# Performance work log

Hardware: AMD Instinct MI355X
Metric: run time of the kernel (lower is better)

Reference implementation:

```python
import jax, jax.numpy as jnp
import numpy as np

N, E, B = 50000, 640000, 4
H, L = 128, 4
NODE_IN, EDGE_IN, COND_IN, NODE_OUT = 12, 4, 10, 3


def _mlp(x, w1, b1, w2, b2):
    # Linear -> ReLU -> Linear
    return jnp.maximum(x @ w1 + b1, 0.0) @ w2 + b2


def setup_inputs() -> dict:
    key = jax.random.key(0)
    keys = iter(jax.random.split(key, 64))

    def p(*shape):
        fan_in = shape[-2] if len(shape) >= 2 else shape[-1]
        return (jax.random.normal(next(keys), shape, jnp.float32) / np.sqrt(fan_in)).astype(jnp.float32)

    inp = {
        "x": jax.random.normal(next(keys), (N, NODE_IN), jnp.float32),
        "edge_index": jax.random.randint(next(keys), (2, E), 0, N),
        "edge_attr": jax.random.normal(next(keys), (E, EDGE_IN), jnp.float32),
        "conditions": jax.random.normal(next(keys), (B, COND_IN), jnp.float32),
        "batch": jnp.sort(jax.random.randint(next(keys), (N,), 0, B)),
        # encoders
        "enc_node_w1": p(NODE_IN, H), "enc_node_b1": jnp.zeros((H,), jnp.float32),
        "enc_node_w2": p(H, H), "enc_node_b2": jnp.zeros((H,), jnp.float32),
        "enc_edge_w1": p(EDGE_IN, H), "enc_edge_b1": jnp.zeros((H,), jnp.float32),
        "enc_edge_w2": p(H, H), "enc_edge_b2": jnp.zeros((H,), jnp.float32),
        "enc_cond_w1": p(COND_IN, H), "enc_cond_b1": jnp.zeros((H,), jnp.float32),
        "enc_cond_w2": p(H, H), "enc_cond_b2": jnp.zeros((H,), jnp.float32),
        # shared MultiheadAttention: with a single key, softmax weight == 1 per head,
        # so output = out_proj(v_proj(kv)); q/k projections cancel exactly (and have
        # identically zero gradient), so only v/out projections are materialized.
        "attn_wv": p(H, H), "attn_bv": jnp.zeros((H,), jnp.float32),
        "attn_wo": p(H, H), "attn_bo": jnp.zeros((H,), jnp.float32),
        # processor layers (stacked over L)
        "pe_w1": p(L, 4 * H, H), "pe_b1": jnp.zeros((L, H), jnp.float32),
        "pe_w2": p(L, H, H), "pe_b2": jnp.zeros((L, H), jnp.float32),
        "pn_w1": p(L, 3 * H, H), "pn_b1": jnp.zeros((L, H), jnp.float32),
        "pn_w2": p(L, H, H), "pn_b2": jnp.zeros((L, H), jnp.float32),
        # decoder
        "dec_w1": p(H, H), "dec_b1": jnp.zeros((H,), jnp.float32),
        "dec_w2": p(H, NODE_OUT), "dec_b2": jnp.zeros((NODE_OUT,), jnp.float32),
    }
    return inp


def reference(x, edge_index, edge_attr, conditions, batch,
              enc_node_w1, enc_node_b1, enc_node_w2, enc_node_b2,
              enc_edge_w1, enc_edge_b1, enc_edge_w2, enc_edge_b2,
              enc_cond_w1, enc_cond_b1, enc_cond_w2, enc_cond_b2,
              attn_wv, attn_bv, attn_wo, attn_bo,
              pe_w1, pe_b1, pe_w2, pe_b2,
              pn_w1, pn_b1, pn_w2, pn_b2,
              dec_w1, dec_b1, dec_w2, dec_b2):
    n = x.shape[0]
    h = _mlp(x, enc_node_w1, enc_node_b1, enc_node_w2, enc_node_b2)           # [N,H]
    e = _mlp(edge_attr, enc_edge_w1, enc_edge_b1, enc_edge_w2, enc_edge_b2)   # [E,H]
    u = _mlp(conditions, enc_cond_w1, enc_cond_b1, enc_cond_w2, enc_cond_b2)  # [B,H]

    row, col = edge_index[0], edge_index[1]
    u_nodes = u[batch]                                                        # [N,H]
    # single-key cross-attention -> softmax over 1 key == 1 -> out_proj(v_proj(u))
    x_cond = (u_nodes @ attn_wv + attn_bv) @ attn_wo + attn_bo               # [N,H], same every layer
    u_edges = u_nodes[row]                                                    # u[batch[row]]

    for l in range(pe_w1.shape[0]):
        # edge update: cat([src, dest, edge_attr, u[batch_e]]) -> MLP
        e = _mlp(jnp.concatenate([h[row], h[col], e, u_edges], axis=1),
                 pe_w1[l], pe_b1[l], pe_w2[l], pe_b2[l])
        # scatter-add aggregation (index_add on row)
        agg = jax.ops.segment_sum(e, row, num_segments=n)                     # [N,H]
        # node update with residual
        h = h + _mlp(jnp.concatenate([h, agg, x_cond], axis=1),
                     pn_w1[l], pn_b1[l], pn_w2[l], pn_b2[l])

    return _mlp(h, dec_w1, dec_b1, dec_w2, dec_b2)                            # [N,node_out]
```

## Files before the change

### kernel.cpp

```cpp
#include <hip/hip_runtime.h>
#include <cstddef>

#define NN 50000
#define NNP 50048
#define NE 640000
#define NB 4
#define H  128
#define NL 4
#define TE 64

typedef unsigned int u32;
typedef unsigned short u16;
typedef __attribute__((ext_vector_type(8))) short bf16x8;
typedef __attribute__((ext_vector_type(4))) float f32x4;

__device__ __forceinline__ float bf2f(u16 s) {
    union { u32 u; float f; } v; v.u = ((u32)s) << 16; return v.f;
}
__device__ __forceinline__ u16 f2bf(float f) {
    union { float f; u32 u; } v; v.f = f;
    u32 u = v.u;
    u += 0x7FFF + ((u >> 16) & 1);
    return (u16)(u >> 16);
}
__device__ __forceinline__ void unpack8(uint4 raw, float* d) {
    d[0] = bf2f(raw.x & 0xFFFF); d[1] = bf2f(raw.x >> 16);
    d[2] = bf2f(raw.y & 0xFFFF); d[3] = bf2f(raw.y >> 16);
    d[4] = bf2f(raw.z & 0xFFFF); d[5] = bf2f(raw.z >> 16);
    d[6] = bf2f(raw.w & 0xFFFF); d[7] = bf2f(raw.w >> 16);
}
__device__ __forceinline__ bf16x8 ld_f32_bf8(const float* __restrict__ p) {
    const float4 a = *(const float4*)p;
    const float4 b = *(const float4*)(p + 4);
    bf16x8 r;
    r[0] = (short)f2bf(a.x); r[1] = (short)f2bf(a.y);
    r[2] = (short)f2bf(a.z); r[3] = (short)f2bf(a.w);
    r[4] = (short)f2bf(b.x); r[5] = (short)f2bf(b.y);
    r[6] = (short)f2bf(b.z); r[7] = (short)f2bf(b.w);
    return r;
}

__global__ __launch_bounds__(256) void k_zero(float* __restrict__ p, int n4) {
    const int i = blockIdx.x * 256 + threadIdx.x;
    if (i < n4) ((float4*)p)[i] = make_float4(0.f, 0.f, 0.f, 0.f);
}

__global__ __launch_bounds__(256) void k_prep(
    const float* __restrict__ pe_w1, const float* __restrict__ pe_w2,
    const float* __restrict__ pn_w1, const float* __restrict__ pn_w2,
    const float* __restrict__ ew2,   const float* __restrict__ nw2,
    u16* __restrict__ W1t, u16* __restrict__ W2t,
    u16* __restrict__ WaT, u16* __restrict__ WbT,
    u16* __restrict__ Wn1aT, u16* __restrict__ Wn1bT, u16* __restrict__ Wn2T,
    u16* __restrict__ W2et, u16* __restrict__ W2nt) {
    const int li = blockIdx.x;
    const float* src; u16* dst;
    switch (blockIdx.y) {
        case 0: src = pe_w1 + ((size_t)li * 512 + 256) * H; dst = W1t  + (size_t)li * H * H; break;
        case 1: src = pe_w2 + (size_t)li * H * H;           dst = W2t  + (size_t)li * H * H; break;
        case 2: src = pe_w1 + (size_t)li * 512 * H;         dst = WaT  + (size_t)li * H * H; break;
        case 3: src = pe_w1 + ((size_t)li * 512 + 128) * H; dst = WbT  + (size_t)li * H * H; break;
        case 4: src = pn_w1 + (size_t)li * 384 * H;         dst = Wn1aT + (size_t)li * H * H; break;
        case 5: src = pn_w1 + ((size_t)li * 384 + 128) * H; dst = Wn1bT + (size_t)li * H * H; break;
        case 6: src = pn_w2 + (size_t)li * H * H;           dst = Wn2T + (size_t)li * H * H; break;
        default:
            if (li == 0)      { src = ew2; dst = W2et; }
            else if (li == 1) { src = nw2; dst = W2nt; }
            else return;
            break;
    }
    for (int idx = threadIdx.x; idx < H * H; idx += 256) {
        const int n = idx >> 7, k = idx & 127;
        dst[idx] = f2bf(src[(size_t)k * H + n]);
    }
}

__global__ __launch_bounds__(128) void k_small(
    const float* __restrict__ cond,
    const float* __restrict__ ecw1, const float* __restrict__ ecb1,
    const float* __restrict__ ecw2, const float* __restrict__ ecb2,
    const float* __restrict__ wv, const float* __restrict__ bv,
    const float* __restrict__ wo, const float* __restrict__ bo,
    const float* __restrict__ pe_w1, const float* __restrict__ pe_b1,
    const float* __restrict__ pn_w1, const float* __restrict__ pn_b1,
    float* __restrict__ cbat, float* __restrict__ nbat) {
    __shared__ float tmp[NB][H];
    __shared__ float uL[NB][H];
    __shared__ float xcL[NB][H];
    const int t = threadIdx.x;
    for (int b = 0; b < NB; ++b) {
        float a = ecb1[t];
        for (int k = 0; k < 10; ++k) a = fmaf(cond[b * 10 + k], ecw1[k * H + t], a);
        tmp[b][t] = fmaxf(a, 0.f);
    }
    __syncthreads();
    for (int b = 0; b < NB; ++b) {
        float a = ecb2[t];
        for (int k = 0; k < H; ++k) a = fmaf(tmp[b][k], ecw2[k * H + t], a);
        uL[b][t] = a;
    }
    __syncthreads();
    for (int b = 0; b < NB; ++b) {
        float a = bv[t];
        for (int k = 0; k < H; ++k) a = fmaf(uL[b][k], wv[k * H + t], a);
        tmp[b][t] = a;
    }
    __syncthreads();
    for (int b = 0; b < NB; ++b) {
        float a = bo[t];
        for (int k = 0; k < H; ++k) a = fmaf(tmp[b][k], wo[k * H + t], a);
        xcL[b][t] = a;
    }
    __syncthreads();
    for (int l = 0; l < NL; ++l) {
        const float* w1u = pe_w1 + ((size_t)l * 512 + 384) * H;
        for (int b = 0; b < NB; ++b) {
            float a = pe_b1[l * H + t];
            for (int k = 0; k < H; ++k) a = fmaf(uL[b][k], w1u[k * H + t], a);
            cbat[(l * NB + b) * H + t] = a;
        }
        const float* w1x = pn_w1 + ((size_t)l * 384 + 256) * H;
        for (int b = 0; b < NB; ++b) {
            float a = pn_b1[l * H + t];
            for (int k = 0; k < H; ++k) a = fmaf(xcL[b][k], w1x[k * H + t], a);
            nbat[(l * NB + b) * H + t] = a;
        }
    }
}

__global__ __launch_bounds__(128) void k_dec_n(
    const float* __restrict__ h,
    const float* __restrict__ w1, const float* __restrict__ b1,
    const float* __restrict__ w2, const float* __restrict__ b2,
    float* __restrict__ out) {
    __shared__ float hid[H];
    const int t = threadIdx.x;
    const long long n = blockIdx.x;
    float a = b1[t];
    for (int k = 0; k < H; ++k) a = fmaf(h[n * H + k], w1[k * H + t], a);
    hid[t] = fmaxf(a, 0.f);
    __syncthreads();
    if (t < 3) {
        float v = b2[t];
        for (int k = 0; k < H; ++k) v = fmaf(hid[k], w2[k * 3 + t], v);
        out[n * 3 + t] = v;
    }
}

__global__ __launch_bounds__(256) void k_enc_e_mfma(
    const float* __restrict__ ea,
    const float* __restrict__ w1, const float* __restrict__ b1,
    const u16* __restrict__ W2et, const float* __restrict__ b2,
    u16* __restrict__ e) {
    __shared__ float SI[TE][H + 4];
    const int t = threadIdx.x;
    const long long e0 = (long long)blockIdx.x * TE;
    const int w = t >> 6, l = t & 63;
    const int m16 = l & 15, g = l >> 4;
    const int row = w * 16 + m16;

    const float4 av = *(const float4*)&ea[(size_t)(e0 + row) * 4];

    bf16x8 afrag[4];
#pragma unroll
    for (int ks = 0; ks < 4; ++ks) {
        const int c0 = ks * 32 + g * 8;
        float hv[8];
        {
            const float4 ba = *(const float4*)&b1[c0];
            const float4 bb = *(const float4*)&b1[c0 + 4];
            hv[0] = ba.x; hv[1] = ba.y; hv[2] = ba.z; hv[3] = ba.w;
            hv[4] = bb.x; hv[5] = bb.y; hv[6] = bb.z; hv[7] = bb.w;
        }
#pragma unroll
        for (int k = 0; k < 4; ++k) {
            const float s = (k == 0) ? av.x : (k == 1) ? av.y : (k == 2) ? av.z : av.w;
            const float4 wa = *(const float4*)&w1[k * H + c0];
            const float4 wb = *(const float4*)&w1[k * H + c0 + 4];
            hv[0] = fmaf(s, wa.x, hv[0]); hv[1] = fmaf(s, wa.y, hv[1]);
            hv[2] = fmaf(s, wa.z, hv[2]); hv[3] = fmaf(s, wa.w, hv[3]);
            hv[4] = fmaf(s, wb.x, hv[4]); hv[5] = fmaf(s, wb.y, hv[5]);
            hv[6] = fmaf(s, wb.z, hv[6]); hv[7] = fmaf(s, wb.w, hv[7]);
        }
#pragma unroll
        for (int j = 0; j < 8; ++j) afrag[ks][j] = (short)f2bf(fmaxf(hv[j], 0.f));
    }

    f32x4 acc[8];
#pragma unroll
    for (int nt = 0; nt < 8; ++nt) {
        const float bb = b2[nt * 16 + m16];
        acc[nt][0] = bb; acc[nt][1] = bb; acc[nt][2] = bb; acc[nt][3] = bb;
    }
#pragma unroll
    for (int ks = 0; ks < 4; ++ks) {
#pragma unroll
        for (int nt = 0; nt < 8; ++nt) {
            const bf16x8 bfr =
                *(const bf16x8*)&W2et[(size_t)(nt * 16 + m16) * H + ks * 32 + g * 8];
            acc[nt] = __builtin_amdgcn_mfma_f32_16x16x32_bf16(afrag[ks], bfr, acc[nt], 0, 0, 0);
        }
    }

#pragma unroll
    for (int nt = 0; nt < 8; ++nt)
#pragma unroll
        for (int j = 0; j < 4; ++j)
            SI[w * 16 + g * 4 + j][nt * 16 + m16] = acc[nt][j];
    __syncthreads();
    for (int u = t; u < TE * 16; u += 256) {
        const int j = u >> 4, c8 = (u & 15) * 8;
        const float* sp = &SI[j][c8];
        uint4 pk;
        pk.x = (u32)f2bf(sp[0]) | ((u32)f2bf(sp[1]) << 16);
        pk.y = (u32)f2bf(sp[2]) | ((u32)f2bf(sp[3]) << 16);
        pk.z = (u32)f2bf(sp[4]) | ((u32)f2bf(sp[5]) << 16);
        pk.w = (u32)f2bf(sp[6]) | ((u32)f2bf(sp[7]) << 16);
        *(uint4*)&e[(size_t)(e0 + j) * H + c8] = pk;
    }
}

__global__ __launch_bounds__(256) void k_enc_n_mfma(
    const float* __restrict__ x,
    const float* __restrict__ w1, const float* __restrict__ b1,
    const u16* __restrict__ W2nt, const float* __restrict__ b2,
    float* __restrict__ h) {
    __shared__ float SI[TE][H + 4];
    const int t = threadIdx.x;
    const long long n0 = (long long)blockIdx.x * TE;
    const int w = t >> 6, l = t & 63;
    const int m16 = l & 15, g = l >> 4;
    const int row = w * 16 + m16;
    const long long nr = (n0 + row < NN) ? (n0 + row) : (NN - 1);

    float av[12];
    {
        const float4 a0 = *(const float4*)&x[nr * 12];
        const float4 a1 = *(const float4*)&x[nr * 12 + 4];
        const float4 a2 = *(const float4*)&x[nr * 12 + 8];
        av[0] = a0.x; av[1] = a0.y; av[2] = a0.z; av[3] = a0.w;
        av[4] = a1.x; av[5] = a1.y; av[6] = a1.z; av[7] = a1.w;
        av[8] = a2.x; av[9] = a2.y; av[10] = a2.z; av[11] = a2.w;
    }

    bf16x8 afrag[4];
#pragma unroll
    for (int ks = 0; ks < 4; ++ks) {
        const int c0 = ks * 32 + g * 8;
        float hv[8];
        {
            const float4 ba = *(const float4*)&b1[c0];
            const float4 bb = *(const float4*)&b1[c0 + 4];
            hv[0] = ba.x; hv[1] = ba.y; hv[2] = ba.z; hv[3] = ba.w;
            hv[4] = bb.x; hv[5] = bb.y; hv[6] = bb.z; hv[7] = bb.w;
        }
#pragma unroll
        for (int k = 0; k < 12; ++k) {
            const float s = av[k];
            const float4 wa = *(const float4*)&w1[k * H + c0];
            const float4 wb = *(const float4*)&w1[k * H + c0 + 4];
            hv[0] = fmaf(s, wa.x, hv[0]); hv[1] = fmaf(s, wa.y, hv[1]);
            hv[2] = fmaf(s, wa.z, hv[2]); hv[3] = fmaf(s, wa.w, hv[3]);
            hv[4] = fmaf(s, wb.x, hv[4]); hv[5] = fmaf(s, wb.y, hv[5]);
            hv[6] = fmaf(s, wb.z, hv[6]); hv[7] = fmaf(s, wb.w, hv[7]);
        }
#pragma unroll
        for (int j = 0; j < 8; ++j) afrag[ks][j] = (short)f2bf(fmaxf(hv[j], 0.f));
    }

    f32x4 acc[8];
#pragma unroll
    for (int nt = 0; nt < 8; ++nt) {
        const float bb = b2[nt * 16 + m16];
        acc[nt][0] = bb; acc[nt][1] = bb; acc[nt][2] = bb; acc[nt][3] = bb;
    }
#pragma unroll
    for (int ks = 0; ks < 4; ++ks) {
#pragma unroll
        for (int nt = 0; nt < 8; ++nt) {
            const bf16x8 bfr =
                *(const bf16x8*)&W2nt[(size_t)(nt * 16 + m16) * H + ks * 32 + g * 8];
            acc[nt] = __builtin_amdgcn_mfma_f32_16x16x32_bf16(afrag[ks], bfr, acc[nt], 0, 0, 0);
        }
    }

#pragma unroll
    for (int nt = 0; nt < 8; ++nt)
#pragma unroll
        for (int j = 0; j < 4; ++j)
            SI[w * 16 + g * 4 + j][nt * 16 + m16] = acc[nt][j];
    __syncthreads();
    for (int u = t; u < TE * H / 4; u += 256) {
        const int j = u >> 5, c4 = (u & 31) * 4;
        *(float4*)&h[(size_t)(n0 + j) * H + c4] = *(const float4*)&SI[j][c4];
    }
}

__global__ __launch_bounds__(256) void k_gemm_dual_mfma(
    const float* __restrict__ h,
    const u16* __restrict__ WaT, const u16* __restrict__ WbT,
    u16* __restrict__ Ca, u16* __restrict__ Cb) {
    __shared__ float SI[TE][H + 4];
    const int t = threadIdx.x;
    const long long n0 = (long long)blockIdx.x * TE;
    const int w = t >> 6, l = t & 63;
    const int m16 = l & 15, g = l >> 4;
    const int row = w * 16 + m16;

    bf16x8 afrag[4];
    {
        const float* hp = h + (size_t)(n0 + row) * H + g * 8;
#pragma unroll
        for (int ks = 0; ks < 4; ++ks) afrag[ks] = ld_f32_bf8(hp + ks * 32);
    }

    f32x4 accA[8], accB[8];
#pragma unroll
    for (int nt = 0; nt < 8; ++nt) {
        accA[nt][0] = 0.f; accA[nt][1] = 0.f; accA[nt][2] = 0.f; accA[nt][3] = 0.f;
        accB[nt][0] = 0.f; accB[nt][1] = 0.f; accB[nt][2] = 0.f; accB[nt][3] = 0.f;
    }
#pragma unroll
    for (int ks = 0; ks < 4; ++ks) {
#pragma unroll
        for (int nt = 0; nt < 8; ++nt) {
            const size_t off = (size_t)(nt * 16 + m16) * H + ks * 32 + g * 8;
            const bf16x8 ba = *(const bf16x8*)&WaT[off];
            const bf16x8 bb = *(const bf16x8*)&WbT[off];
            accA[nt] = __builtin_amdgcn_mfma_f32_16x16x32_bf16(afrag[ks], ba, accA[nt], 0, 0, 0);
            accB[nt] = __builtin_amdgcn_mfma_f32_16x16x32_bf16(afrag[ks], bb, accB[nt], 0, 0, 0);
        }
    }

#pragma unroll
    for (int s = 0; s < 2; ++s) {
        __syncthreads();
#pragma unroll
        for (int nt = 0; nt < 8; ++nt)
#pragma unroll
            for (int j = 0; j < 4; ++j)
                SI[w * 16 + g * 4 + j][nt * 16 + m16] = s ? accB[nt][j] : accA[nt][j];
        __syncthreads();
        u16* C = s ? Cb : Ca;
        for (int u = t; u < TE * 16; u += 256) {
            const int j = u >> 4, c8 = (u & 15) * 8;
            const float* sp = &SI[j][c8];
            uint4 pk;
            pk.x = (u32)f2bf(sp[0]) | ((u32)f2bf(sp[1]) << 16);
            pk.y = (u32)f2bf(sp[2]) | ((u32)f2bf(sp[3]) << 16);
            pk.z = (u32)f2bf(sp[4]) | ((u32)f2bf(sp[5]) << 16);
            pk.w = (u32)f2bf(sp[6]) | ((u32)f2bf(sp[7]) << 16);
            *(uint4*)&C[(size_t)(n0 + j) * H + c8] = pk;
        }
    }
}

__global__ __launch_bounds__(256) void k_edge_mfma(
    const u16* __restrict__ hA, const u16* __restrict__ hB,
    const float* __restrict__ cbatl,
    const u16* __restrict__ W1t, const u16* __restrict__ W2t,
    const float* __restrict__ b2,
    const int* __restrict__ rowi, const int* __restrict__ coli,
    const int* __restrict__ batch,
    u16* __restrict__ e, float* __restrict__ agg) {
    __shared__ float SI[TE][H + 4];
    __shared__ int rL[TE], cL[TE], bL[TE];
    const int t = threadIdx.x;
    const long long e0 = (long long)blockIdx.x * TE;

    if (t < TE) {
        const int r = rowi[e0 + t];
        rL[t] = r; bL[t] = batch[r];
    } else if (t < 2 * TE) {
        cL[t - TE] = coli[e0 + t - TE];
    }
    __syncthreads();

    for (int u = t; u < TE * 16; u += 256) {
        const int j = u >> 4, c8 = (u & 15) * 8;
        float va[8], vb[8];
        unpack8(*(const uint4*)&hA[(size_t)rL[j] * H + c8], va);
        unpack8(*(const uint4*)&hB[(size_t)cL[j] * H + c8], vb);
        const float* cb = &cbatl[bL[j] * H + c8];
#pragma unroll
        for (int q = 0; q < 8; ++q) SI[j][c8 + q] = va[q] + vb[q] + cb[q];
    }

    const int w = t >> 6, l = t & 63;
    const int m16 = l & 15, g = l >> 4;

    bf16x8 afrag[4];
    {
        const u16* ep = e + (size_t)(e0 + w * 16 + m16) * H + g * 8;
#pragma unroll
        for (int ks = 0; ks < 4; ++ks) afrag[ks] = *(const bf16x8*)(ep + ks * 32);
    }
    __syncthreads();

    f32x4 acc[8];
#pragma unroll
    for (int nt = 0; nt < 8; ++nt) {
#pragma unroll
        for (int j = 0; j < 4; ++j)
            acc[nt][j] = SI[w * 16 + g * 4 + j][nt * 16 + m16];
#pragma unroll
        for (int ks = 0; ks < 4; ++ks) {
            const bf16x8 bfr =
                *(const bf16x8*)&W1t[(size_t)(nt * 16 + m16) * H + ks * 32 + g * 8];
            acc[nt] = __builtin_amdgcn_mfma_f32_16x16x32_bf16(afrag[ks], bfr, acc[nt], 0, 0, 0);
        }
    }
    __syncthreads();

#pragma unroll
    for (int nt = 0; nt < 8; ++nt)
#pragma unroll
        for (int j = 0; j < 4; ++j)
            SI[w * 16 + g * 4 + j][nt * 16 + m16] = fmaxf(acc[nt][j], 0.f);
    __syncthreads();

    f32x4 acc2[8];
#pragma unroll
    for (int nt = 0; nt < 8; ++nt) {
        const float bb = b2[nt * 16 + m16];
        acc2[nt][0] = bb; acc2[nt][1] = bb; acc2[nt][2] = bb; acc2[nt][3] = bb;
    }
#pragma unroll
    for (int ks = 0; ks < 4; ++ks) {
        bf16x8 a2;
        const float* hp = &SI[w * 16 + m16][ks * 32 + g * 8];
#pragma unroll
        for (int j = 0; j < 8; ++j) a2[j] = (short)f2bf(hp[j]);
#pragma unroll
        for (int nt = 0; nt < 8; ++nt) {
            const bf16x8 bfr =
                *(const bf16x8*)&W2t[(size_t)(nt * 16 + m16) * H + ks * 32 + g * 8];
            acc2[nt] = __builtin_amdgcn_mfma_f32_16x16x32_bf16(a2, bfr, acc2[nt], 0, 0, 0);
        }
    }
    __syncthreads();

#pragma unroll
    for (int nt = 0; nt < 8; ++nt)
#pragma unroll
        for (int j = 0; j < 4; ++j)
            SI[w * 16 + g * 4 + j][nt * 16 + m16] = acc2[nt][j];
    __syncthreads();

    for (int u = t; u < TE * 16; u += 256) {
        const int j = u >> 4, c8 = (u & 15) * 8;
        const float* sp = &SI[j][c8];
        uint4 pk;
        pk.x = (u32)f2bf(sp[0]) | ((u32)f2bf(sp[1]) << 16);
        pk.y = (u32)f2bf(sp[2]) | ((u32)f2bf(sp[3]) << 16);
        pk.z = (u32)f2bf(sp[4]) | ((u32)f2bf(sp[5]) << 16);
        pk.w = (u32)f2bf(sp[6]) | ((u32)f2bf(sp[7]) << 16);
        *(uint4*)&e[(size_t)(e0 + j) * H + c8] = pk;
    }
    for (int idx = t; idx < TE * H; idx += 256) {
        const int j = idx >> 7, c = idx & 127;
        atomicAdd(&agg[(size_t)rL[j] * H + c], SI[j][c]);
    }
}

__global__ __launch_bounds__(256) void k_node_mfma(
    const u16* __restrict__ Wn1aT, const u16* __restrict__ Wn1bT,
    const u16* __restrict__ Wn2T, const float* __restrict__ bn2,
    const float* __restrict__ nbatl, const int* __restrict__ batch,
    const float* __restrict__ agg, float* __restrict__ h) {
    __shared__ float SI[TE][H + 4];
    __shared__ float NBl[NB][H];
    __shared__ int bL[TE];
    const int t = threadIdx.x;
    const long long n0 = (long long)blockIdx.x * TE;
    if (t < TE) {
        const long long n = n0 + t;
        bL[t] = batch[n < NN ? n : (NN - 1)];
    }
    for (int i = t; i < NB * H; i += 256) ((float*)NBl)[i] = nbatl[i];

    const int w = t >> 6, l = t & 63;
    const int m16 = l & 15, g = l >> 4;
    const int row = w * 16 + m16;

    bf16x8 afrag[4];
    {
        const float* hp = h + (size_t)(n0 + row) * H + g * 8;
#pragma unroll
        for (int ks = 0; ks < 4; ++ks) afrag[ks] = ld_f32_bf8(hp + ks * 32);
    }
    __syncthreads();

    f32x4 acc[8];
#pragma unroll
    for (int nt = 0; nt < 8; ++nt)
#pragma unroll
        for (int j = 0; j < 4; ++j)
            acc[nt][j] = NBl[bL[w * 16 + g * 4 + j]][nt * 16 + m16];

#pragma unroll
    for (int ks = 0; ks < 4; ++ks)
#pragma unroll
        for (int nt = 0; nt < 8; ++nt) {
            const bf16x8 bfr =
                *(const bf16x8*)&Wn1aT[(size_t)(nt * 16 + m16) * H + ks * 32 + g * 8];
            acc[nt] = __builtin_amdgcn_mfma_f32_16x16x32_bf16(afrag[ks], bfr, acc[nt], 0, 0, 0);
        }

    {
        const float* ap = agg + (size_t)(n0 + row) * H + g * 8;
#pragma unroll
        for (int ks = 0; ks < 4; ++ks) afrag[ks] = ld_f32_bf8(ap + ks * 32);
    }
#pragma unroll
    for (int ks = 0; ks < 4; ++ks)
#pragma unroll
        for (int nt = 0; nt < 8; ++nt) {
            const bf16x8 bfr =
                *(const bf16x8*)&Wn1bT[(size_t)(nt * 16 + m16) * H + ks * 32 + g * 8];
            acc[nt] = __builtin_amdgcn_mfma_f32_16x16x32_bf16(afrag[ks], bfr, acc[nt], 0, 0, 0);
        }

#pragma unroll
    for (int nt = 0; nt < 8; ++nt)
#pragma unroll
        for (int j = 0; j < 4; ++j)
            SI[w * 16 + g * 4 + j][nt * 16 + m16] = fmaxf(acc[nt][j], 0.f);
    __syncthreads();

    f32x4 acc2[8];
#pragma unroll
    for (int nt = 0; nt < 8; ++nt) {
        const float bb = bn2[nt * 16 + m16];
        acc2[nt][0] = bb; acc2[nt][1] = bb; acc2[nt][2] = bb; acc2[nt][3] = bb;
    }
#pragma unroll
    for (int ks = 0; ks < 4; ++ks) {
        bf16x8 a2;
        const float* hp = &SI[w * 16 + m16][ks * 32 + g * 8];
#pragma unroll
        for (int j = 0; j < 8; ++j) a2[j] = (short)f2bf(hp[j]);
#pragma unroll
        for (int nt = 0; nt < 8; ++nt) {
            const bf16x8 bfr =
                *(const bf16x8*)&Wn2T[(size_t)(nt * 16 + m16) * H + ks * 32 + g * 8];
            acc2[nt] = __builtin_amdgcn_mfma_f32_16x16x32_bf16(a2, bfr, acc2[nt], 0, 0, 0);
        }
    }
    __syncthreads();

#pragma unroll
    for (int nt = 0; nt < 8; ++nt)
#pragma unroll
        for (int j = 0; j < 4; ++j)
            SI[w * 16 + g * 4 + j][nt * 16 + m16] = acc2[nt][j];
    __syncthreads();

    for (int u = t; u < TE * H / 4; u += 256) {
        const int j = u >> 5, c4 = (u & 31) * 4;
        float4 hv = *(const float4*)&h[(size_t)(n0 + j) * H + c4];
        const float4 sv = *(const float4*)&SI[j][c4];
        hv.x += sv.x; hv.y += sv.y; hv.z += sv.z; hv.w += sv.w;
        *(float4*)&h[(size_t)(n0 + j) * H + c4] = hv;
    }
}

extern "C" void kernel_launch(void* const* d_in, const int* in_sizes, int n_in,
                              void* d_out, int out_size, void* d_ws, size_t ws_size,
                              hipStream_t stream) {
    const float* x          = (const float*)d_in[0];
    const int*   edge_index = (const int*)d_in[1];
    const float* edge_attr  = (const float*)d_in[2];
    const float* cond       = (const float*)d_in[3];
    const int*   batch      = (const int*)d_in[4];
    const float* enc_node_w1 = (const float*)d_in[5];
    const float* enc_node_b1 = (const float*)d_in[6];
    const float* enc_node_w2 = (const float*)d_in[7];
    const float* enc_node_b2 = (const float*)d_in[8];
    const float* enc_edge_w1 = (const float*)d_in[9];
    const float* enc_edge_b1 = (const float*)d_in[10];
    const float* enc_edge_w2 = (const float*)d_in[11];
    const float* enc_edge_b2 = (const float*)d_in[12];
    const float* enc_cond_w1 = (const float*)d_in[13];
    const float* enc_cond_b1 = (const float*)d_in[14];
    const float* enc_cond_w2 = (const float*)d_in[15];
    const float* enc_cond_b2 = (const float*)d_in[16];
    const float* attn_wv = (const float*)d_in[17];
    const float* attn_bv = (const float*)d_in[18];
    const float* attn_wo = (const float*)d_in[19];
    const float* attn_bo = (const float*)d_in[20];
    const float* pe_w1 = (const float*)d_in[21];
    const float* pe_b1 = (const float*)d_in[22];
    const float* pe_w2 = (const float*)d_in[23];
    const float* pe_b2 = (const float*)d_in[24];
    const float* pn_w1 = (const float*)d_in[25];
    const float* pn_b1 = (const float*)d_in[26];
    const float* pn_w2 = (const float*)d_in[27];
    const float* pn_b2 = (const float*)d_in[28];
    const float* dec_w1 = (const float*)d_in[29];
    const float* dec_b1 = (const float*)d_in[30];
    const float* dec_w2 = (const float*)d_in[31];
    const float* dec_b2 = (const float*)d_in[32];

    u16*   e    = (u16*)d_ws;
    float* h    = (float*)((char*)d_ws + (size_t)NE * H * 2);
    float* agg  = h + (size_t)NNP * H;
    u16*   hA   = (u16*)(agg + (size_t)NNP * H);
    u16*   hB   = hA + (size_t)NNP * H;
    float* cbat = (float*)(hB + (size_t)NNP * H);
    float* nbat = cbat + NL * NB * H;
    u16*   W1t   = (u16*)(nbat + NL * NB * H);
    u16*   W2t   = W1t  + (size_t)NL * H * H;
    u16*   WaT   = W2t  + (size_t)NL * H * H;
    u16*   WbT   = WaT  + (size_t)NL * H * H;
    u16*   Wn1aT = WbT  + (size_t)NL * H * H;
    u16*   Wn1bT = Wn1aT + (size_t)NL * H * H;
    u16*   Wn2T  = Wn1bT + (size_t)NL * H * H;
    u16*   W2et  = Wn2T + (size_t)NL * H * H;
    u16*   W2nt  = W2et + (size_t)H * H;

    const int* rowi = edge_index;
    const int* coli = edge_index + NE;
    float* out = (float*)d_out;

    k_prep<<<dim3(NL, 8), 256, 0, stream>>>(pe_w1, pe_w2, pn_w1, pn_w2,
                                            enc_edge_w2, enc_node_w2,
                                            W1t, W2t, WaT, WbT,
                                            Wn1aT, Wn1bT, Wn2T, W2et, W2nt);
    k_small<<<1, 128, 0, stream>>>(cond, enc_cond_w1, enc_cond_b1, enc_cond_w2, enc_cond_b2,
                                   attn_wv, attn_bv, attn_wo, attn_bo,
                                   pe_w1, pe_b1, pn_w1, pn_b1, cbat, nbat);
    k_enc_n_mfma<<<NNP / TE, 256, 0, stream>>>(
        x, enc_node_w1, enc_node_b1, W2nt, enc_node_b2, h);
    k_enc_e_mfma<<<NE / TE, 256, 0, stream>>>(
        edge_attr, enc_edge_w1, enc_edge_b1, W2et, enc_edge_b2, e);

    for (int l = 0; l < NL; ++l) {
        k_zero<<<(NNP * H / 4 + 255) / 256, 256, 0, stream>>>(agg, NNP * H / 4);
        k_gemm_dual_mfma<<<NNP / TE, 256, 0, stream>>>(h, WaT + (size_t)l * H * H,
                                                       WbT + (size_t)l * H * H, hA, hB);
        k_edge_mfma<<<NE / TE, 256, 0, stream>>>(
            hA, hB, cbat + l * NB * H,
            W1t + (size_t)l * H * H, W2t + (size_t)l * H * H,
            pe_b2 + l * H, rowi, coli, batch, e, agg);
        k_node_mfma<<<NNP / TE, 256, 0, stream>>>(
            Wn1aT + (size_t)l * H * H, Wn1bT + (size_t)l * H * H,
            Wn2T + (size_t)l * H * H, pn_b2 + l * H,
            nbat + l * NB * H, batch, agg, h);
    }
    k_dec_n<<<NN, 128, 0, stream>>>(h, dec_w1, dec_b1, dec_w2, dec_b2, out);
}
```

Baseline: 2.448 ms.

## Sort edges by destination row, pre-reduce scatter-adds, MFMA decoder, skip final edge write

Builds a counting-sort permutation of the edges by source row (histogram, scan, scatter) and processes edges in that order. This lets the edge kernel sum consecutive same-row contributions inside a block before issuing atomics, which cuts atomic traffic into agg. The last layer's edge kernel no longer writes e, since nothing reads it afterwards. The per-node scalar decoder is replaced by a tiled MFMA kernel. In exchange the code adds a few preprocessing launches and an indirect gather through the permutation, and the node-dependent atomic ordering changes floating-point summation order.

```diff
diff --git a/kernel.cpp b/kernel.cpp
--- a/kernel.cpp
+++ b/kernel.cpp
@@ -45,14 +45,51 @@
     if (i < n4) ((float4*)p)[i] = make_float4(0.f, 0.f, 0.f, 0.f);
 }
 
+__global__ __launch_bounds__(256) void k_hist(const int* __restrict__ rowi,
+                                              u32* __restrict__ cnt) {
+    const int i = blockIdx.x * 256 + threadIdx.x;
+    if (i < NE) atomicAdd(&cnt[rowi[i]], 1u);
+}
+
+__global__ __launch_bounds__(1024) void k_scan(u32* __restrict__ cnt) {
+    __shared__ u32 part[1024];
+    const int t = threadIdx.x;
+    const int CHUNK = (NN + 1023) / 1024;
+    const int lo = t * CHUNK;
+    const int hi = (lo + CHUNK < NN) ? lo + CHUNK : NN;
+    u32 s = 0;
+    for (int i = lo; i < hi; ++i) s += cnt[i];
+    part[t] = s;
+    __syncthreads();
+    for (int ofs = 1; ofs < 1024; ofs <<= 1) {
+        const u32 v = (t >= ofs) ? part[t - ofs] : 0u;
+        __syncthreads();
+        part[t] += v;
+        __syncthreads();
+    }
+    u32 run = (t == 0) ? 0u : part[t - 1];
+    for (int i = lo; i < hi; ++i) { const u32 c = cnt[i]; cnt[i] = run; run += c; }
+}
+
+__global__ __launch_bounds__(256) void k_scatter(const int* __restrict__ rowi,
+                                                 u32* __restrict__ off,
+                                                 int* __restrict__ permS) {
+    const int i = blockIdx.x * 256 + threadIdx.x;
+    if (i < NE) {
+        const u32 p = atomicAdd(&off[rowi[i]], 1u);
+        permS[p] = i;
+    }
+}
+
 __global__ __launch_bounds__(256) void k_prep(
     const float* __restrict__ pe_w1, const float* __restrict__ pe_w2,
     const float* __restrict__ pn_w1, const float* __restrict__ pn_w2,
     const float* __restrict__ ew2,   const float* __restrict__ nw2,
+    const float* __restrict__ dw1,
     u16* __restrict__ W1t, u16* __restrict__ W2t,
     u16* __restrict__ WaT, u16* __restrict__ WbT,
     u16* __restrict__ Wn1aT, u16* __restrict__ Wn1bT, u16* __restrict__ Wn2T,
-    u16* __restrict__ W2et, u16* __restrict__ W2nt) {
+    u16* __restrict__ W2et, u16* __restrict__ W2nt, u16* __restrict__ W1dt) {
     const int li = blockIdx.x;
     const float* src; u16* dst;
     switch (blockIdx.y) {
@@ -66,6 +103,7 @@
         default:
             if (li == 0)      { src = ew2; dst = W2et; }
             else if (li == 1) { src = nw2; dst = W2nt; }
+            else if (li == 2) { src = dw1; dst = W1dt; }
             else return;
             break;
     }
@@ -128,27 +166,9 @@
     }
 }
 
-__global__ __launch_bounds__(128) void k_dec_n(
-    const float* __restrict__ h,
-    const float* __restrict__ w1, const float* __restrict__ b1,
-    const float* __restrict__ w2, const float* __restrict__ b2,
-    float* __restrict__ out) {
-    __shared__ float hid[H];
-    const int t = threadIdx.x;
-    const long long n = blockIdx.x;
-    float a = b1[t];
-    for (int k = 0; k < H; ++k) a = fmaf(h[n * H + k], w1[k * H + t], a);
-    hid[t] = fmaxf(a, 0.f);
-    __syncthreads();
-    if (t < 3) {
-        float v = b2[t];
-        for (int k = 0; k < H; ++k) v = fmaf(hid[k], w2[k * 3 + t], v);
-        out[n * 3 + t] = v;
-    }
-}
-
 __global__ __launch_bounds__(256) void k_enc_e_mfma(
     const float* __restrict__ ea,
+    const int* __restrict__ permS,
     const float* __restrict__ w1, const float* __restrict__ b1,
     const u16* __restrict__ W2et, const float* __restrict__ b2,
     u16* __restrict__ e) {
@@ -159,7 +179,8 @@
     const int m16 = l & 15, g = l >> 4;
     const int row = w * 16 + m16;
 
-    const float4 av = *(const float4*)&ea[(size_t)(e0 + row) * 4];
+    const int src = permS[e0 + row];
+    const float4 av = *(const float4*)&ea[(size_t)src * 4];
 
     bf16x8 afrag[4];
 #pragma unroll
@@ -355,13 +376,14 @@
     }
 }
 
+template <bool WRITE_E>
 __global__ __launch_bounds__(256) void k_edge_mfma(
     const u16* __restrict__ hA, const u16* __restrict__ hB,
     const float* __restrict__ cbatl,
     const u16* __restrict__ W1t, const u16* __restrict__ W2t,
     const float* __restrict__ b2,
     const int* __restrict__ rowi, const int* __restrict__ coli,
-    const int* __restrict__ batch,
+    const int* __restrict__ batch, const int* __restrict__ permS,
     u16* __restrict__ e, float* __restrict__ agg) {
     __shared__ float SI[TE][H + 4];
     __shared__ int rL[TE], cL[TE], bL[TE];
@@ -369,10 +391,9 @@
     const long long e0 = (long long)blockIdx.x * TE;
 
     if (t < TE) {
-        const int r = rowi[e0 + t];
-        rL[t] = r; bL[t] = batch[r];
-    } else if (t < 2 * TE) {
-        cL[t - TE] = coli[e0 + t - TE];
+        const int p = permS[e0 + t];
+        const int r = rowi[p];
+        rL[t] = r; cL[t] = coli[p]; bL[t] = batch[r];
     }
     __syncthreads();
 
@@ -447,19 +468,33 @@
             SI[w * 16 + g * 4 + j][nt * 16 + m16] = acc2[nt][j];
     __syncthreads();
 
-    for (int u = t; u < TE * 16; u += 256) {
-        const int j = u >> 4, c8 = (u & 15) * 8;
-        const float* sp = &SI[j][c8];
-        uint4 pk;
-        pk.x = (u32)f2bf(sp[0]) | ((u32)f2bf(sp[1]) << 16);
-        pk.y = (u32)f2bf(sp[2]) | ((u32)f2bf(sp[3]) << 16);
-        pk.z = (u32)f2bf(sp[4]) | ((u32)f2bf(sp[5]) << 16);
-        pk.w = (u32)f2bf(sp[6]) | ((u32)f2bf(sp[7]) << 16);
-        *(uint4*)&e[(size_t)(e0 + j) * H + c8] = pk;
-    }
-    for (int idx = t; idx < TE * H; idx += 256) {
-        const int j = idx >> 7, c = idx & 127;
-        atomicAdd(&agg[(size_t)rL[j] * H + c], SI[j][c]);
+    if (WRITE_E) {
+        for (int u = t; u < TE * 16; u += 256) {
+            const int j = u >> 4, c8 = (u & 15) * 8;
+            const float* sp = &SI[j][c8];
+            uint4 pk;
+            pk.x = (u32)f2bf(sp[0]) | ((u32)f2bf(sp[1]) << 16);
+            pk.y = (u32)f2bf(sp[2]) | ((u32)f2bf(sp[3]) << 16);
+            pk.z = (u32)f2bf(sp[4]) | ((u32)f2bf(sp[5]) << 16);
+            pk.w = (u32)f2bf(sp[6]) | ((u32)f2bf(sp[7]) << 16);
+            *(uint4*)&e[(size_t)(e0 + j) * H + c8] = pk;
+        }
+    }
+
+    {
+        const int c = t & 127;
+        const int j0 = (t >> 7) * 32;
+        float sum = SI[j0][c];
+        int prev = rL[j0];
+        for (int j = j0 + 1; j < j0 + 32; ++j) {
+            const int r = rL[j];
+            if (r != prev) {
+                atomicAdd(&agg[(size_t)prev * H + c], sum);
+                sum = 0.f; prev = r;
+            }
+            sum += SI[j][c];
+        }
+        atomicAdd(&agg[(size_t)prev * H + c], sum);
     }
 }
 
@@ -562,6 +597,58 @@
         const float4 sv = *(const float4*)&SI[j][c4];
         hv.x += sv.x; hv.y += sv.y; hv.z += sv.z; hv.w += sv.w;
         *(float4*)&h[(size_t)(n0 + j) * H + c4] = hv;
+    }
+}
+
+__global__ __launch_bounds__(256) void k_dec_mfma(
+    const float* __restrict__ h,
+    const u16* __restrict__ W1dt, const float* __restrict__ b1,
+    const float* __restrict__ w2, const float* __restrict__ b2,
+    float* __restrict__ out) {
+    __shared__ float SI[TE][H + 4];
+    const int t = threadIdx.x;
+    const long long n0 = (long long)blockIdx.x * TE;
+    const int w = t >> 6, l = t & 63;
+    const int m16 = l & 15, g = l >> 4;
+    const int row = w * 16 + m16;
+
+    bf16x8 afrag[4];
+    {
+        const float* hp = h + (size_t)(n0 + row) * H + g * 8;
+#pragma unroll
+        for (int ks = 0; ks < 4; ++ks) afrag[ks] = ld_f32_bf8(hp + ks * 32);
+    }
+
+    f32x4 acc[8];
+#pragma unroll
+    for (int nt = 0; nt < 8; ++nt) {
+        const float bb = b1[nt * 16 + m16];
+        acc[nt][0] = bb; acc[nt][1] = bb; acc[nt][2] = bb; acc[nt][3] = bb;
+    }
+#pragma unroll
+    for (int ks = 0; ks < 4; ++ks) {
+#pragma unroll
+        for (int nt = 0; nt < 8; ++nt) {
+            const bf16x8 bfr =
+                *(const bf16x8*)&W1dt[(size_t)(nt * 16 + m16) * H + ks * 32 + g * 8];
+            acc[nt] = __builtin_amdgcn_mfma_f32_16x16x32_bf16(afrag[ks], bfr, acc[nt], 0, 0, 0);
+        }
+    }
+
+#pragma unroll
+    for (int nt = 0; nt < 8; ++nt)
+#pragma unroll
+        for (int j = 0; j < 4; ++j)
+            SI[w * 16 + g * 4 + j][nt * 16 + m16] = fmaxf(acc[nt][j], 0.f);
+    __syncthreads();
+
+    if (t < TE * 3) {
+        const int n = t / 3, c = t - n * 3;
+        if (n0 + n < NN) {
+            float v = b2[c];
+            for (int k = 0; k < H; ++k) v = fmaf(SI[n][k], w2[k * 3 + c], v);
+            out[(size_t)(n0 + n) * 3 + c] = v;
+        }
     }
 }
 
@@ -618,35 +705,49 @@
     u16*   Wn2T  = Wn1bT + (size_t)NL * H * H;
     u16*   W2et  = Wn2T + (size_t)NL * H * H;
     u16*   W2nt  = W2et + (size_t)H * H;
+    u16*   W1dt  = W2nt + (size_t)H * H;
+    u32*   cnt   = (u32*)(W1dt + (size_t)H * H);
+    int*   permS = (int*)(cnt + NNP);
 
     const int* rowi = edge_index;
     const int* coli = edge_index + NE;
     float* out = (float*)d_out;
 
+    k_zero<<<(NNP / 4 + 255) / 256, 256, 0, stream>>>((float*)cnt, NNP / 4);
+    k_hist<<<NE / 256, 256, 0, stream>>>(rowi, cnt);
+    k_scan<<<1, 1024, 0, stream>>>(cnt);
+    k_scatter<<<NE / 256, 256, 0, stream>>>(rowi, cnt, permS);
+
     k_prep<<<dim3(NL, 8), 256, 0, stream>>>(pe_w1, pe_w2, pn_w1, pn_w2,
-                                            enc_edge_w2, enc_node_w2,
+                                            enc_edge_w2, enc_node_w2, dec_w1,
                                             W1t, W2t, WaT, WbT,
-                                            Wn1aT, Wn1bT, Wn2T, W2et, W2nt);
+                                            Wn1aT, Wn1bT, Wn2T, W2et, W2nt, W1dt);
     k_small<<<1, 128, 0, stream>>>(cond, enc_cond_w1, enc_cond_b1, enc_cond_w2, enc_cond_b2,
                                    attn_wv, attn_bv, attn_wo, attn_bo,
                                    pe_w1, pe_b1, pn_w1, pn_b1, cbat, nbat);
     k_enc_n_mfma<<<NNP / TE, 256, 0, stream>>>(
         x, enc_node_w1, enc_node_b1, W2nt, enc_node_b2, h);
     k_enc_e_mfma<<<NE / TE, 256, 0, stream>>>(
-        edge_attr, enc_edge_w1, enc_edge_b1, W2et, enc_edge_b2, e);
+        edge_attr, permS, enc_edge_w1, enc_edge_b1, W2et, enc_edge_b2, e);
 
     for (int l = 0; l < NL; ++l) {
         k_zero<<<(NNP * H / 4 + 255) / 256, 256, 0, stream>>>(agg, NNP * H / 4);
         k_gemm_dual_mfma<<<NNP / TE, 256, 0, stream>>>(h, WaT + (size_t)l * H * H,
                                                        WbT + (size_t)l * H * H, hA, hB);
-        k_edge_mfma<<<NE / TE, 256, 0, stream>>>(
-            hA, hB, cbat + l * NB * H,
-            W1t + (size_t)l * H * H, W2t + (size_t)l * H * H,
-            pe_b2 + l * H, rowi, coli, batch, e, agg);
+        if (l < NL - 1)
+            k_edge_mfma<true><<<NE / TE, 256, 0, stream>>>(
+                hA, hB, cbat + l * NB * H,
+                W1t + (size_t)l * H * H, W2t + (size_t)l * H * H,
+                pe_b2 + l * H, rowi, coli, batch, permS, e, agg);
+        else
+            k_edge_mfma<false><<<NE / TE, 256, 0, stream>>>(
+                hA, hB, cbat + l * NB * H,
+                W1t + (size_t)l * H * H, W2t + (size_t)l * H * H,
+                pe_b2 + l * H, rowi, coli, batch, permS, e, agg);
         k_node_mfma<<<NNP / TE, 256, 0, stream>>>(
             Wn1aT + (size_t)l * H * H, Wn1bT + (size_t)l * H * H,
             Wn2T + (size_t)l * H * H, pn_b2 + l * H,
             nbat + l * NB * H, batch, agg, h);
     }
-    k_dec_n<<<NN, 128, 0, stream>>>(h, dec_w1, dec_b1, dec_w2, dec_b2, out);
-}
+    k_dec_mfma<<<NNP / TE, 256, 0, stream>>>(h, W1dt, dec_b1, dec_w2, dec_b2, out);
+}
```

After: 2.485 ms. No clear change (+1.5%).
